# Optimization experiments

Measured on AMD Instinct MI355X. Metric: run time of the kernel, lower is better.

Reference implementation:

```python
import jax, jax.numpy as jnp
import numpy as np

B, S, H = 8, 2048, 256

def setup_inputs() -> dict:
    key = jax.random.key(0)
    ks = jax.random.split(key, 6)
    scale = 1.0 / np.sqrt(H)
    return {
        "query": jax.random.normal(ks[0], (B, S, H), dtype=jnp.float32),
        "key_in": jax.random.normal(ks[1], (B, S, H), dtype=jnp.float32),
        "value": jax.random.normal(ks[2], (B, S, H), dtype=jnp.float32),
        "Wq": jax.random.uniform(ks[3], (H, H), dtype=jnp.float32, minval=-scale, maxval=scale),
        "Wk": jax.random.uniform(ks[4], (H, H), dtype=jnp.float32, minval=-scale, maxval=scale),
        "Wv": jax.random.uniform(ks[5], (H, H), dtype=jnp.float32, minval=-scale, maxval=scale),
    }

def reference(query, key_in, value, Wq, Wk, Wv):
    # nn.Linear(bias=False): y = x @ W.T
    q = jnp.einsum('bsh,dh->bsd', query, Wq)
    k = jnp.einsum('bsh,dh->bsd', key_in, Wk)
    v = jnp.einsum('bsh,dh->bsd', value, Wv)
    # unscaled attention, exactly as in the torch module
    scores = jnp.einsum('bqd,bkd->bqk', q, k)  # [B, Sq, Skv]
    weights = jax.nn.softmax(scores, axis=-1)
    context = jnp.einsum('bqk,bkd->bqd', weights, v)
    return context
```

## Files before the change

### kernel.cpp

```cpp
#include <hip/hip_runtime.h>
#include <hip/hip_bf16.h>

typedef short short8 __attribute__((ext_vector_type(8)));
typedef _Float16 half8 __attribute__((ext_vector_type(8)));
typedef __fp16 fp16x2 __attribute__((ext_vector_type(2)));
typedef float f32x4  __attribute__((ext_vector_type(4)));
typedef float f32x16 __attribute__((ext_vector_type(16)));

__device__ __forceinline__ unsigned short f2h(float f) {
  _Float16 h = (_Float16)f;
  return __builtin_bit_cast(unsigned short, h);
}
__device__ __forceinline__ half8 as_h8(short8 s) { return __builtin_bit_cast(half8, s); }

__global__ __launch_bounds__(256) void proj_kernel(
    const float* __restrict__ Aq, const float* __restrict__ Bq,
    const float* __restrict__ Ak, const float* __restrict__ Bk,
    const float* __restrict__ Av, const float* __restrict__ Bv,
    short* __restrict__ Cq, short* __restrict__ Ck, short* __restrict__ Cv) {
  __shared__ short At[128][40];
  __shared__ short Bt[128][40];
  const int y = blockIdx.y;
  const float* A  = (y == 0) ? Aq : (y == 1) ? Ak : Av;
  const float* Bm = (y == 0) ? Bq : (y == 1) ? Bk : Bv;
  short* C        = (y == 0) ? Cq : (y == 1) ? Ck : Cv;
  const int mode = (y == 2);
  const float scale = (y == 0) ? 1.44269504f : 1.0f;
  const int x = blockIdx.x;
  const int batch = x & 7, loc = (x >> 3) & 15, half = x >> 7;
  int m0, n0;
  if (!mode) { m0 = (batch * 16 + loc) * 128; n0 = half * 128; }
  else       { m0 = half * 128; n0 = (batch * 16 + loc) * 128; }

  const int t = threadIdx.x;
  const int w = t >> 6, l = t & 63;
  const int wr = (w >> 1) * 64, wc = (w & 1) * 64;
  f32x4 acc[4][4] = {};
  for (int k0 = 0; k0 < 256; k0 += 32) {
    __syncthreads();
    #pragma unroll
    for (int rep = 0; rep < 4; ++rep) {
      int row = (t >> 3) + rep * 32;
      int c4  = (t & 7) * 4;
      float4 va = *(const float4*)(A + (size_t)(m0 + row) * 256 + k0 + c4);
      unsigned long long pa = (unsigned long long)f2h(va.x) |
                              ((unsigned long long)f2h(va.y) << 16) |
                              ((unsigned long long)f2h(va.z) << 32) |
                              ((unsigned long long)f2h(va.w) << 48);
      *(unsigned long long*)&At[row][c4] = pa;
      float4 vb = *(const float4*)(Bm + (size_t)(n0 + row) * 256 + k0 + c4);
      unsigned long long pb = (unsigned long long)f2h(vb.x) |
                              ((unsigned long long)f2h(vb.y) << 16) |
                              ((unsigned long long)f2h(vb.z) << 32) |
                              ((unsigned long long)f2h(vb.w) << 48);
      *(unsigned long long*)&Bt[row][c4] = pb;
    }
    __syncthreads();
    short8 af[4], bf[4];
    #pragma unroll
    for (int i = 0; i < 4; ++i) {
      af[i] = *(const short8*)&At[wr + i * 16 + (l & 15)][(l >> 4) * 8];
      bf[i] = *(const short8*)&Bt[wc + i * 16 + (l & 15)][(l >> 4) * 8];
    }
    #pragma unroll
    for (int i = 0; i < 4; ++i)
      #pragma unroll
      for (int j = 0; j < 4; ++j)
        acc[i][j] = __builtin_amdgcn_mfma_f32_16x16x32_f16(as_h8(af[i]), as_h8(bf[j]),
                                                           acc[i][j], 0, 0, 0);
  }
  #pragma unroll
  for (int i = 0; i < 4; ++i)
    #pragma unroll
    for (int j = 0; j < 4; ++j)
      #pragma unroll
      for (int r = 0; r < 4; ++r) {
        int row = m0 + wr + i * 16 + (l >> 4) * 4 + r;
        int col = n0 + wc + j * 16 + (l & 15);
        size_t idx;
        if (!mode) {
          int b = row >> 11, s = row & 2047;
          int T = s >> 5, ln = s & 31;
          int kf = col >> 4, g = (col >> 3) & 1, jj = col & 7;
          idx = (((size_t)(b * 64 + T) * 16 + kf) * 64 + g * 32 + ln) * 8 + jj;
        } else {
          int b = col >> 11, s = col & 2047;
          int T = s >> 5, k2 = (s >> 4) & 1, g = (s >> 3) & 1, jj = s & 7;
          int db = row >> 5, ln = row & 31;
          idx = ((((size_t)(b * 64 + T) * 2 + k2) * 8 + db) * 64 + g * 32 + ln) * 8 + jj;
        }
        C[idx] = (short)f2h(acc[i][j][r] * scale);
      }
}

__global__ __launch_bounds__(512, 4) void attn_kernel(const short* __restrict__ QP,
                                                      const short* __restrict__ KP,
                                                      const short* __restrict__ VP,
                                                      float* __restrict__ O) {
  __shared__ __align__(16) char arena[16384 + 20480 + 1024 + 1024];
  short* Qlds = (short*)arena;
  short (*Plds)[32][40] = (short (*)[32][40])(arena + 16384);
  float (*mx_sh)[8] = (float (*)[8])(arena + 16384 + 20480);
  float (*l_sh)[8]  = (float (*)[8])(arena + 16384 + 20480 + 1024);
  float (*tbuf)[32][33] = (float (*)[32][33])arena;

  const int t = threadIdx.x;
  const int w = t >> 6, l = t & 63;
  const int q = l & 31, grp = l >> 5;
  const int bid = blockIdx.x;
  const int b = bid & 7;
  const int q0 = (bid >> 3) * 32;
  const size_t bS = (size_t)b * 2048;

  const short* kptr = KP + (((size_t)(b * 64 + w)) << 13) + l * 8;
  const short* vptr = VP + (((size_t)(b * 64)) << 13) + ((size_t)w << 9) + l * 8;

  short8 ka[8];
  #pragma unroll
  for (int j = 0; j < 8; ++j) ka[j] = *(const short8*)(kptr + j * 512);

  {
    const short* qsrc = QP + ((size_t)(b * 64 + (q0 >> 5)) * 16) * 512;
    *(short8*)&Qlds[t * 8] = *(const short8*)(qsrc + t * 8);
    *(short8*)&Qlds[(t + 512) * 8] = *(const short8*)(qsrc + (t + 512) * 8);
  }
  __syncthreads();

  f32x16 ot0 = {}, ot1 = {};
  float m = -1e30f, lsum = 0.f;

  for (int it = 0; it < 8; ++it) {
    const short* kb = kptr + ((size_t)it << 16);
    f32x16 st0 = {}, st1 = {};
    __builtin_amdgcn_s_setprio(1);
    #pragma unroll
    for (int j = 0; j < 8; ++j) {
      short8 a1 = *(const short8*)(kb + (8 + j) * 512);
      short8 qa = *(const short8*)&Qlds[j * 512 + l * 8];
      short8 qb = *(const short8*)&Qlds[(8 + j) * 512 + l * 8];
      st0 = __builtin_amdgcn_mfma_f32_32x32x16_f16(as_h8(ka[j]), as_h8(qa), st0, 0, 0, 0);
      st1 = __builtin_amdgcn_mfma_f32_32x32x16_f16(as_h8(a1), as_h8(qb), st1, 0, 0, 0);
    }
    __builtin_amdgcn_s_setprio(0);
    #pragma unroll
    for (int j = 0; j < 8; ++j) ka[j] = *(const short8*)(kb + 65536 + j * 512);

    f32x16 st = st0 + st1;

    float xa = fmaxf(fmaxf(fmaxf(st[0], st[1]), fmaxf(st[2], st[3])),
                     fmaxf(fmaxf(st[4], st[5]), fmaxf(st[6], st[7])));
    float xb = fmaxf(fmaxf(fmaxf(st[8], st[9]), fmaxf(st[10], st[11])),
                     fmaxf(fmaxf(st[12], st[13]), fmaxf(st[14], st[15])));
    float tmax = fmaxf(xa, xb);
    tmax = fmaxf(tmax, __shfl_xor(tmax, 32, 64));
    if (l < 32) mx_sh[q][w] = tmax;
    __syncthreads();

    f32x4 mA = *(const f32x4*)&mx_sh[q][0];
    f32x4 mB = *(const f32x4*)&mx_sh[q][4];
    float t8 = fmaxf(fmaxf(fmaxf(mA[0], mA[1]), fmaxf(mA[2], mA[3])),
                     fmaxf(fmaxf(mB[0], mB[1]), fmaxf(mB[2], mB[3])));

    if (!__all(t8 - m <= 11.544f)) {
      float mnew = fmaxf(m, t8);
      float corr = exp2f(m - mnew);
      lsum *= corr;
      ot0 *= corr;
      ot1 *= corr;
      m = mnew;
    }

    #pragma unroll
    for (int r = 0; r < 16; ++r) st[r] = exp2f(st[r] - m);
    float s0 = (st[0] + st[1]) + (st[2] + st[3]);
    float s1 = (st[4] + st[5]) + (st[6] + st[7]);
    float s2 = (st[8] + st[9]) + (st[10] + st[11]);
    float s3 = (st[12] + st[13]) + (st[14] + st[15]);
    float psum = (s0 + s1) + (s2 + s3);
    psum += __shfl_xor(psum, 32, 64);
    lsum += psum;

    #pragma unroll
    for (int i = 0; i < 8; ++i) {
      fp16x2 pk = __builtin_amdgcn_cvt_pkrtz(st[2 * i], st[2 * i + 1]);
      int kvb = ((2 * i) & 3) + 8 * (i >> 1) + 4 * grp;
      *(unsigned*)&Plds[w][q][kvb] = __builtin_bit_cast(unsigned, pk);
    }
    __syncthreads();

    const short* vb = vptr + ((size_t)it << 16);
    __builtin_amdgcn_s_setprio(1);
    #pragma unroll
    for (int s = 0; s < 8; ++s) {
      short8 pb0 = *(const short8*)&Plds[s][q][grp * 8];
      short8 pb1 = *(const short8*)&Plds[s][q][16 + grp * 8];
      short8 vf0 = *(const short8*)(vb + s * 8192);
      short8 vf1 = *(const short8*)(vb + s * 8192 + 4096);
      ot0 = __builtin_amdgcn_mfma_f32_32x32x16_f16(as_h8(vf0), as_h8(pb0), ot0, 0, 0, 0);
      ot1 = __builtin_amdgcn_mfma_f32_32x32x16_f16(as_h8(vf1), as_h8(pb1), ot1, 0, 0, 0);
    }
    __builtin_amdgcn_s_setprio(0);
  }

  if (l < 32) l_sh[q][w] = lsum;
  __syncthreads();
  f32x4 lA = *(const f32x4*)&l_sh[q][0];
  f32x4 lB = *(const f32x4*)&l_sh[q][4];
  float Ltot = ((lA[0] + lA[1]) + (lA[2] + lA[3])) + ((lB[0] + lB[1]) + (lB[2] + lB[3]));
  float invL = 1.0f / Ltot;

  #pragma unroll
  for (int r = 0; r < 16; ++r)
    tbuf[w][(r & 3) + 8 * (r >> 2) + 4 * grp][q] = (ot0[r] + ot1[r]) * invL;
  #pragma unroll
  for (int rr = 0; rr < 16; ++rr) {
    int qq = grp + rr * 2;
    O[(bS + q0 + qq) * 256 + w * 32 + q] = tbuf[w][q][qq];
  }
}

extern "C" void kernel_launch(void* const* d_in, const int* in_sizes, int n_in,
                              void* d_out, int out_size, void* d_ws, size_t ws_size,
                              hipStream_t stream) {
  (void)in_sizes; (void)n_in; (void)out_size; (void)ws_size;
  const float* query  = (const float*)d_in[0];
  const float* key_in = (const float*)d_in[1];
  const float* value  = (const float*)d_in[2];
  const float* Wq     = (const float*)d_in[3];
  const float* Wk     = (const float*)d_in[4];
  const float* Wv     = (const float*)d_in[5];
  float* out = (float*)d_out;

  short* q_ws = (short*)d_ws;
  short* k_ws = q_ws + (size_t)16384 * 256;
  short* v_ws = k_ws + (size_t)16384 * 256;

  dim3 gp(256, 3), ga(512);
  proj_kernel<<<gp, 256, 0, stream>>>(query, Wq, key_in, Wk, Wv, value,
                                      q_ws, k_ws, v_ws);
  attn_kernel<<<ga, 512, 0, stream>>>(q_ws, k_ws, v_ws, out);
}
```

Before: 82.18 us.

## Double query tile per block to 64 rows with 16 waves sharing K/V

The attention kernel now processes 64 query rows per block with 1024 threads (16 waves) instead of 32 rows with 512 threads, halving the grid. Each pair of waves shares K and V fragments across two query halves, with separate running maxima per half, so K/V global traffic per query is reduced. The K register prefetch across iterations is dropped and K is loaded inline, LDS use doubles, and occupancy per CU may fall under launch_bounds(1024,4).

```diff
diff --git a/kernel.cpp b/kernel.cpp
--- a/kernel.cpp
+++ b/kernel.cpp
@@ -93,58 +93,55 @@
       }
 }
 
-__global__ __launch_bounds__(512, 4) void attn_kernel(const short* __restrict__ QP,
-                                                      const short* __restrict__ KP,
-                                                      const short* __restrict__ VP,
-                                                      float* __restrict__ O) {
-  __shared__ __align__(16) char arena[16384 + 20480 + 1024 + 1024];
+__global__ __launch_bounds__(1024, 4) void attn_kernel(const short* __restrict__ QP,
+                                                       const short* __restrict__ KP,
+                                                       const short* __restrict__ VP,
+                                                       float* __restrict__ O) {
+  __shared__ __align__(16) char arena[32768 + 40960 + 2048 + 2048];
   short* Qlds = (short*)arena;
-  short (*Plds)[32][40] = (short (*)[32][40])(arena + 16384);
-  float (*mx_sh)[8] = (float (*)[8])(arena + 16384 + 20480);
-  float (*l_sh)[8]  = (float (*)[8])(arena + 16384 + 20480 + 1024);
+  short (*Plds)[32][40] = (short (*)[32][40])(arena + 32768);
+  float (*mx_sh)[8] = (float (*)[8])(arena + 32768 + 40960);
+  float (*l_sh)[8]  = (float (*)[8])(arena + 32768 + 40960 + 2048);
   float (*tbuf)[32][33] = (float (*)[32][33])arena;
 
   const int t = threadIdx.x;
   const int w = t >> 6, l = t & 63;
   const int q = l & 31, grp = l >> 5;
+  const int wq = w >> 3, wkv = w & 7;
+  const int wd = w >> 1, pvh = w & 1;
   const int bid = blockIdx.x;
   const int b = bid & 7;
-  const int q0 = (bid >> 3) * 32;
+  const int q0 = (bid >> 3) * 64;
   const size_t bS = (size_t)b * 2048;
-
-  const short* kptr = KP + (((size_t)(b * 64 + w)) << 13) + l * 8;
-  const short* vptr = VP + (((size_t)(b * 64)) << 13) + ((size_t)w << 9) + l * 8;
-
-  short8 ka[8];
-  #pragma unroll
-  for (int j = 0; j < 8; ++j) ka[j] = *(const short8*)(kptr + j * 512);
 
   {
     const short* qsrc = QP + ((size_t)(b * 64 + (q0 >> 5)) * 16) * 512;
     *(short8*)&Qlds[t * 8] = *(const short8*)(qsrc + t * 8);
-    *(short8*)&Qlds[(t + 512) * 8] = *(const short8*)(qsrc + (t + 512) * 8);
+    *(short8*)&Qlds[(t + 1024) * 8] = *(const short8*)(qsrc + (t + 1024) * 8);
   }
   __syncthreads();
 
+  const short* kptr = KP + (((size_t)(b * 64 + wkv)) << 13) + l * 8;
+  const short* vptr = VP + (((size_t)(b * 64)) << 13) + ((size_t)wd << 9) + l * 8;
+  const short* qh   = Qlds + (wq << 13) + l * 8;
+
   f32x16 ot0 = {}, ot1 = {};
-  float m = -1e30f, lsum = 0.f;
+  float m_a = -1e30f, m_b = -1e30f, lsum = 0.f;
 
   for (int it = 0; it < 8; ++it) {
     const short* kb = kptr + ((size_t)it << 16);
     f32x16 st0 = {}, st1 = {};
     __builtin_amdgcn_s_setprio(1);
     #pragma unroll
-    for (int j = 0; j < 8; ++j) {
-      short8 a1 = *(const short8*)(kb + (8 + j) * 512);
-      short8 qa = *(const short8*)&Qlds[j * 512 + l * 8];
-      short8 qb = *(const short8*)&Qlds[(8 + j) * 512 + l * 8];
-      st0 = __builtin_amdgcn_mfma_f32_32x32x16_f16(as_h8(ka[j]), as_h8(qa), st0, 0, 0, 0);
+    for (int kf = 0; kf < 16; kf += 2) {
+      short8 a0 = *(const short8*)(kb + kf * 512);
+      short8 a1 = *(const short8*)(kb + (kf + 1) * 512);
+      short8 qa = *(const short8*)(qh + kf * 512);
+      short8 qb = *(const short8*)(qh + (kf + 1) * 512);
+      st0 = __builtin_amdgcn_mfma_f32_32x32x16_f16(as_h8(a0), as_h8(qa), st0, 0, 0, 0);
       st1 = __builtin_amdgcn_mfma_f32_32x32x16_f16(as_h8(a1), as_h8(qb), st1, 0, 0, 0);
     }
     __builtin_amdgcn_s_setprio(0);
-    #pragma unroll
-    for (int j = 0; j < 8; ++j) ka[j] = *(const short8*)(kb + 65536 + j * 512);
-
     f32x16 st = st0 + st1;
 
     float xa = fmaxf(fmaxf(fmaxf(st[0], st[1]), fmaxf(st[2], st[3])),
@@ -153,25 +150,33 @@
                      fmaxf(fmaxf(st[12], st[13]), fmaxf(st[14], st[15])));
     float tmax = fmaxf(xa, xb);
     tmax = fmaxf(tmax, __shfl_xor(tmax, 32, 64));
-    if (l < 32) mx_sh[q][w] = tmax;
-    __syncthreads();
-
-    f32x4 mA = *(const f32x4*)&mx_sh[q][0];
-    f32x4 mB = *(const f32x4*)&mx_sh[q][4];
-    float t8 = fmaxf(fmaxf(fmaxf(mA[0], mA[1]), fmaxf(mA[2], mA[3])),
-                     fmaxf(fmaxf(mB[0], mB[1]), fmaxf(mB[2], mB[3])));
-
-    if (!__all(t8 - m <= 11.544f)) {
-      float mnew = fmaxf(m, t8);
-      float corr = exp2f(m - mnew);
-      lsum *= corr;
-      ot0 *= corr;
-      ot1 *= corr;
-      m = mnew;
-    }
-
-    #pragma unroll
-    for (int r = 0; r < 16; ++r) st[r] = exp2f(st[r] - m);
+    if (l < 32) mx_sh[wq * 32 + q][wkv] = tmax;
+    __syncthreads();
+
+    f32x4 aA = *(const f32x4*)&mx_sh[q][0];
+    f32x4 aB = *(const f32x4*)&mx_sh[q][4];
+    float t8a = fmaxf(fmaxf(fmaxf(aA[0], aA[1]), fmaxf(aA[2], aA[3])),
+                      fmaxf(fmaxf(aB[0], aB[1]), fmaxf(aB[2], aB[3])));
+    f32x4 bA = *(const f32x4*)&mx_sh[32 + q][0];
+    f32x4 bB = *(const f32x4*)&mx_sh[32 + q][4];
+    float t8b = fmaxf(fmaxf(fmaxf(bA[0], bA[1]), fmaxf(bA[2], bA[3])),
+                      fmaxf(fmaxf(bB[0], bB[1]), fmaxf(bB[2], bB[3])));
+
+    bool ok = (t8a - m_a <= 11.544f) && (t8b - m_b <= 11.544f);
+    if (!__all(ok)) {
+      float na = fmaxf(m_a, t8a), nb = fmaxf(m_b, t8b);
+      float ca = exp2f(m_a - na), cb = exp2f(m_b - nb);
+      float cpv = pvh ? cb : ca;
+      ot0 *= cpv;
+      ot1 *= cpv;
+      lsum *= (wq ? cb : ca);
+      m_a = na;
+      m_b = nb;
+    }
+    float mm = wq ? m_b : m_a;
+
+    #pragma unroll
+    for (int r = 0; r < 16; ++r) st[r] = exp2f(st[r] - mm);
     float s0 = (st[0] + st[1]) + (st[2] + st[3]);
     float s1 = (st[4] + st[5]) + (st[6] + st[7]);
     float s2 = (st[8] + st[9]) + (st[10] + st[11]);
@@ -184,7 +189,7 @@
     for (int i = 0; i < 8; ++i) {
       fp16x2 pk = __builtin_amdgcn_cvt_pkrtz(st[2 * i], st[2 * i + 1]);
       int kvb = ((2 * i) & 3) + 8 * (i >> 1) + 4 * grp;
-      *(unsigned*)&Plds[w][q][kvb] = __builtin_bit_cast(unsigned, pk);
+      *(unsigned*)&Plds[wkv * 2 + wq][q][kvb] = __builtin_bit_cast(unsigned, pk);
     }
     __syncthreads();
 
@@ -192,8 +197,8 @@
     __builtin_amdgcn_s_setprio(1);
     #pragma unroll
     for (int s = 0; s < 8; ++s) {
-      short8 pb0 = *(const short8*)&Plds[s][q][grp * 8];
-      short8 pb1 = *(const short8*)&Plds[s][q][16 + grp * 8];
+      short8 pb0 = *(const short8*)&Plds[s * 2 + pvh][q][grp * 8];
+      short8 pb1 = *(const short8*)&Plds[s * 2 + pvh][q][16 + grp * 8];
       short8 vf0 = *(const short8*)(vb + s * 8192);
       short8 vf1 = *(const short8*)(vb + s * 8192 + 4096);
       ot0 = __builtin_amdgcn_mfma_f32_32x32x16_f16(as_h8(vf0), as_h8(pb0), ot0, 0, 0, 0);
@@ -202,10 +207,10 @@
     __builtin_amdgcn_s_setprio(0);
   }
 
-  if (l < 32) l_sh[q][w] = lsum;
+  if (l < 32) l_sh[wq * 32 + q][wkv] = lsum;
   __syncthreads();
-  f32x4 lA = *(const f32x4*)&l_sh[q][0];
-  f32x4 lB = *(const f32x4*)&l_sh[q][4];
+  f32x4 lA = *(const f32x4*)&l_sh[pvh * 32 + q][0];
+  f32x4 lB = *(const f32x4*)&l_sh[pvh * 32 + q][4];
   float Ltot = ((lA[0] + lA[1]) + (lA[2] + lA[3])) + ((lB[0] + lB[1]) + (lB[2] + lB[3]));
   float invL = 1.0f / Ltot;
 
@@ -215,7 +220,7 @@
   #pragma unroll
   for (int rr = 0; rr < 16; ++rr) {
     int qq = grp + rr * 2;
-    O[(bS + q0 + qq) * 256 + w * 32 + q] = tbuf[w][q][qq];
+    O[(bS + q0 + pvh * 32 + qq) * 256 + wd * 32 + q] = tbuf[w][q][qq];
   }
 }
 
@@ -235,8 +240,8 @@
   short* k_ws = q_ws + (size_t)16384 * 256;
   short* v_ws = k_ws + (size_t)16384 * 256;
 
-  dim3 gp(256, 3), ga(512);
+  dim3 gp(256, 3), ga(256);
   proj_kernel<<<gp, 256, 0, stream>>>(query, Wq, key_in, Wk, Wv, value,
                                       q_ws, k_ws, v_ws);
-  attn_kernel<<<ga, 512, 0, stream>>>(q_ws, k_ws, v_ws, out);
-}
+  attn_kernel<<<ga, 1024, 0, stream>>>(q_ws, k_ws, v_ws, out);
+}
```

After: 85.43 us. 1.04x slower.

## Split attention KV range in two with log-sum-exp merge kernel

Applied to the files above, without the earlier changes.

Splits the key/value sequence into two halves processed by separate blocks (1024 blocks instead of 512), each writing a partial normalized output plus a log-sum-exp statistic, then adds a merge kernel that combines the halves. The aim is more parallelism and occupancy on the GPU's many CUs, with launch bounds raised to 8 waves per SIMD. It drops the register prefetch of K fragments and adds a third kernel launch plus extra global traffic for the fp16 partial output and the merge pass; storing the second half in fp16 slightly reduces precision.

```diff
diff --git a/kernel.cpp b/kernel.cpp
--- a/kernel.cpp
+++ b/kernel.cpp
@@ -93,10 +93,12 @@
       }
 }
 
-__global__ __launch_bounds__(512, 4) void attn_kernel(const short* __restrict__ QP,
+__global__ __launch_bounds__(512, 8) void attn_kernel(const short* __restrict__ QP,
                                                       const short* __restrict__ KP,
                                                       const short* __restrict__ VP,
-                                                      float* __restrict__ O) {
+                                                      float* __restrict__ O0,
+                                                      short* __restrict__ O1,
+                                                      float* __restrict__ sws) {
   __shared__ __align__(16) char arena[16384 + 20480 + 1024 + 1024];
   short* Qlds = (short*)arena;
   short (*Plds)[32][40] = (short (*)[32][40])(arena + 16384);
@@ -108,16 +110,13 @@
   const int w = t >> 6, l = t & 63;
   const int q = l & 31, grp = l >> 5;
   const int bid = blockIdx.x;
+  const int kvh = bid >> 9;
   const int b = bid & 7;
-  const int q0 = (bid >> 3) * 32;
+  const int q0 = ((bid >> 3) & 63) * 32;
   const size_t bS = (size_t)b * 2048;
 
-  const short* kptr = KP + (((size_t)(b * 64 + w)) << 13) + l * 8;
-  const short* vptr = VP + (((size_t)(b * 64)) << 13) + ((size_t)w << 9) + l * 8;
-
-  short8 ka[8];
-  #pragma unroll
-  for (int j = 0; j < 8; ++j) ka[j] = *(const short8*)(kptr + j * 512);
+  const short* kptr = KP + (((size_t)(b * 64 + kvh * 32 + w)) << 13) + l * 8;
+  const short* vptr = VP + (((size_t)(b * 64 + kvh * 32)) << 13) + ((size_t)w << 9) + l * 8;
 
   {
     const short* qsrc = QP + ((size_t)(b * 64 + (q0 >> 5)) * 16) * 512;
@@ -129,22 +128,20 @@
   f32x16 ot0 = {}, ot1 = {};
   float m = -1e30f, lsum = 0.f;
 
-  for (int it = 0; it < 8; ++it) {
+  for (int it = 0; it < 4; ++it) {
     const short* kb = kptr + ((size_t)it << 16);
     f32x16 st0 = {}, st1 = {};
     __builtin_amdgcn_s_setprio(1);
     #pragma unroll
-    for (int j = 0; j < 8; ++j) {
-      short8 a1 = *(const short8*)(kb + (8 + j) * 512);
-      short8 qa = *(const short8*)&Qlds[j * 512 + l * 8];
-      short8 qb = *(const short8*)&Qlds[(8 + j) * 512 + l * 8];
-      st0 = __builtin_amdgcn_mfma_f32_32x32x16_f16(as_h8(ka[j]), as_h8(qa), st0, 0, 0, 0);
+    for (int kf = 0; kf < 16; kf += 2) {
+      short8 a0 = *(const short8*)(kb + kf * 512);
+      short8 a1 = *(const short8*)(kb + (kf + 1) * 512);
+      short8 qa = *(const short8*)&Qlds[kf * 512 + l * 8];
+      short8 qb = *(const short8*)&Qlds[(kf + 1) * 512 + l * 8];
+      st0 = __builtin_amdgcn_mfma_f32_32x32x16_f16(as_h8(a0), as_h8(qa), st0, 0, 0, 0);
       st1 = __builtin_amdgcn_mfma_f32_32x32x16_f16(as_h8(a1), as_h8(qb), st1, 0, 0, 0);
     }
     __builtin_amdgcn_s_setprio(0);
-    #pragma unroll
-    for (int j = 0; j < 8; ++j) ka[j] = *(const short8*)(kb + 65536 + j * 512);
-
     f32x16 st = st0 + st1;
 
     float xa = fmaxf(fmaxf(fmaxf(st[0], st[1]), fmaxf(st[2], st[3])),
@@ -209,14 +206,51 @@
   float Ltot = ((lA[0] + lA[1]) + (lA[2] + lA[3])) + ((lB[0] + lB[1]) + (lB[2] + lB[3]));
   float invL = 1.0f / Ltot;
 
+  if (w == 0 && l < 32)
+    sws[kvh * 16384 + (int)bS + q0 + q] = m + __log2f(Ltot);
+
   #pragma unroll
   for (int r = 0; r < 16; ++r)
     tbuf[w][(r & 3) + 8 * (r >> 2) + 4 * grp][q] = (ot0[r] + ot1[r]) * invL;
-  #pragma unroll
-  for (int rr = 0; rr < 16; ++rr) {
-    int qq = grp + rr * 2;
-    O[(bS + q0 + qq) * 256 + w * 32 + q] = tbuf[w][q][qq];
-  }
+  if (kvh == 0) {
+    #pragma unroll
+    for (int rr = 0; rr < 16; ++rr) {
+      int qq = grp + rr * 2;
+      O0[(bS + q0 + qq) * 256 + w * 32 + q] = tbuf[w][q][qq];
+    }
+  } else {
+    #pragma unroll
+    for (int rr = 0; rr < 16; ++rr) {
+      int qq = grp + rr * 2;
+      O1[(bS + q0 + qq) * 256 + w * 32 + q] = (short)f2h(tbuf[w][q][qq]);
+    }
+  }
+}
+
+__global__ __launch_bounds__(256) void merge_kernel(float* __restrict__ O,
+                                                    const short* __restrict__ O1,
+                                                    const float* __restrict__ sws) {
+  int i = blockIdx.x * 256 + threadIdx.x;
+  int row = i >> 5;
+  float s0 = sws[row], s1 = sws[16384 + row];
+  float mx = fmaxf(s0, s1);
+  float e0 = exp2f(s0 - mx), e1 = exp2f(s1 - mx);
+  float inv = 1.0f / (e0 + e1);
+  float w0 = e0 * inv, w1 = e1 * inv;
+  float4 a0 = *(const float4*)(O + (size_t)i * 8);
+  float4 a1 = *(const float4*)(O + (size_t)i * 8 + 4);
+  half8 h = as_h8(*(const short8*)(O1 + (size_t)i * 8));
+  float4 r0, r1;
+  r0.x = w0 * a0.x + w1 * (float)h[0];
+  r0.y = w0 * a0.y + w1 * (float)h[1];
+  r0.z = w0 * a0.z + w1 * (float)h[2];
+  r0.w = w0 * a0.w + w1 * (float)h[3];
+  r1.x = w0 * a1.x + w1 * (float)h[4];
+  r1.y = w0 * a1.y + w1 * (float)h[5];
+  r1.z = w0 * a1.z + w1 * (float)h[6];
+  r1.w = w0 * a1.w + w1 * (float)h[7];
+  *(float4*)(O + (size_t)i * 8) = r0;
+  *(float4*)(O + (size_t)i * 8 + 4) = r1;
 }
 
 extern "C" void kernel_launch(void* const* d_in, const int* in_sizes, int n_in,
@@ -234,9 +268,12 @@
   short* q_ws = (short*)d_ws;
   short* k_ws = q_ws + (size_t)16384 * 256;
   short* v_ws = k_ws + (size_t)16384 * 256;
-
-  dim3 gp(256, 3), ga(512);
+  short* o1_ws = v_ws + (size_t)16384 * 256;
+  float* s_ws  = (float*)(o1_ws + (size_t)16384 * 256);
+
+  dim3 gp(256, 3), ga(1024), gm(2048);
   proj_kernel<<<gp, 256, 0, stream>>>(query, Wq, key_in, Wk, Wv, value,
                                       q_ws, k_ws, v_ws);
-  attn_kernel<<<ga, 512, 0, stream>>>(q_ws, k_ws, v_ws, out);
-}
+  attn_kernel<<<ga, 512, 0, stream>>>(q_ws, k_ws, v_ws, out, o1_ws, s_ws);
+  merge_kernel<<<gm, 256, 0, stream>>>(out, o1_ws, s_ws);
+}
```

Measured after the change: 127.6 us. +55.3%, slower.
